# Kernel optimization log

Hardware: AMD Instinct MI355X
Metric: run time of the kernel (lower is better)

Reference implementation:

```python
import jax, jax.numpy as jnp
import numpy as np

B, N, D = 8, 2048, 256      # batch, tokens, model dim (= out_token_dims)
S = 128                     # query_key_dims
H = int(2.0 * D)            # expansion_factor * D = 512
EPS = 1e-5


def setup_inputs() -> dict:
    key = jax.random.key(0)
    ks = jax.random.split(key, 4)
    x = jax.random.normal(ks[0], (B, N, D), dtype=jnp.float32)
    g = jnp.ones((), jnp.float32)                                # ScaleNorm gain
    W_uv = jax.random.normal(ks[1], (D, 2 * H + S), jnp.float32) * 0.02
    b_uv = jnp.zeros((2 * H + S,), jnp.float32)
    gamma = jnp.ones((2, S), jnp.float32)                        # OffsetScale scale
    beta = jnp.zeros((2, S), jnp.float32)                        # OffsetScale offset
    W_o = jax.random.normal(ks[2], (H, D), jnp.float32) * 0.02
    b_o = jnp.zeros((D,), jnp.float32)
    return {"x": x, "g": g, "W_uv": W_uv, "b_uv": b_uv,
            "gamma": gamma, "beta": beta, "W_o": W_o, "b_o": b_o}


def reference(x, g, W_uv, b_uv, gamma, beta, W_o, b_o):
    d = x.shape[-1]
    # ScaleNorm: x / max(||x|| / sqrt(d), eps) * g
    norm = jnp.linalg.norm(x, axis=-1, keepdims=True) * jax.lax.rsqrt(jnp.float32(d))
    xn = x / jnp.maximum(norm, EPS) * g
    # fused uv projection + SiLU
    uv = jax.nn.silu(jnp.einsum('bnd,de->bne', xn, W_uv) + b_uv)
    u = uv[..., :H]            # gate branch        [B,N,H]
    v = uv[..., H:2 * H]       # value branch       [B,N,H]
    base = uv[..., 2 * H:]     # shared q/k base    [B,N,S]
    # OffsetScale heads=2 -> q, k (cheap per-dim affine)
    q = base * gamma[0] + beta[0]
    k = base * gamma[1] + beta[1]
    # single-head scores + ReLU^2 attention activation
    qk = jnp.einsum('bns,bms->bnm', q, k) * jax.lax.rsqrt(jnp.float32(S))
    attn = jnp.square(jax.nn.relu(qk))
    # gate * (attn @ v), then output projection back to D
    gated = u * jnp.einsum('bnm,bmh->bnh', attn, v)
    return jnp.einsum('bnh,hd->bnd', gated, W_o) + b_o
```

## Files before the change

kernel.cpp:

```cpp
#include <hip/hip_runtime.h>
#include <math.h>

#define BB 8
#define NN 2048
#define DD 256
#define SS 128
#define HH 512
#define EE 1152

typedef short bf16x8 __attribute__((ext_vector_type(8)));
typedef float f32x4 __attribute__((ext_vector_type(4)));

__device__ __forceinline__ short f2bf(float f) {
    union { float f; unsigned u; } a; a.f = f;
    unsigned r = a.u + 0x7FFFu + ((a.u >> 16) & 1u);
    return (short)(r >> 16);
}
__device__ __forceinline__ float bf2f(short s) {
    union { unsigned u; float f; } a; a.u = ((unsigned)(unsigned short)s) << 16;
    return a.f;
}
__device__ __forceinline__ void gl_lds16(const short* g, short* l) {
    __builtin_amdgcn_global_load_lds(
        (const __attribute__((address_space(1))) void*)g,
        (__attribute__((address_space(3))) void*)l, 16, 0, 0);
}

__global__ __launch_bounds__(256) void k_pre(
        const float* __restrict__ x, const float* __restrict__ gp,
        short* __restrict__ xn,
        const float* __restrict__ Wuv, const float* __restrict__ Wo,
        short* __restrict__ Wuv_t, short* __restrict__ Wo_t) {
    __shared__ float tile[32][33];
    int bid = blockIdx.x;
    int t = threadIdx.x;
    if (bid < 4096) {
        int wave = t >> 6, lane = t & 63;
        long row = (long)bid * 4 + wave;
        float4 xv = ((const float4*)(x + row * DD))[lane];
        float ss = xv.x*xv.x + xv.y*xv.y + xv.z*xv.z + xv.w*xv.w;
        #pragma unroll
        for (int off = 32; off > 0; off >>= 1) ss += __shfl_down(ss, off);
        ss = __shfl(ss, 0);
        float norm = sqrtf(ss) * 0.0625f;
        float scale = gp[0] / fmaxf(norm, 1e-5f);
        short4 o;
        o.x = f2bf(xv.x * scale); o.y = f2bf(xv.y * scale);
        o.z = f2bf(xv.z * scale); o.w = f2bf(xv.w * scale);
        ((short4*)(xn + row * DD))[lane] = o;
    } else if (bid < 4384) {
        int bid2 = bid - 4096;
        int et = bid2 % 36, dt = bid2 / 36;
        #pragma unroll
        for (int i = 0; i < 4; i++) {
            int idx = t + i*256, r = idx >> 5, c = idx & 31;
            tile[r][c] = Wuv[(long)(dt*32 + r)*EE + et*32 + c];
        }
        __syncthreads();
        #pragma unroll
        for (int i = 0; i < 4; i++) {
            int idx = t + i*256, r = idx >> 5, c = idx & 31;
            Wuv_t[(long)(et*32 + r)*DD + dt*32 + c] = f2bf(tile[c][r]);
        }
    } else {
        int bid3 = bid - 4384;
        int ht = bid3 % 16, dt = bid3 / 16;
        #pragma unroll
        for (int i = 0; i < 4; i++) {
            int idx = t + i*256, r = idx >> 5, c = idx & 31;
            tile[r][c] = Wo[(long)(ht*32 + r)*DD + dt*32 + c];
        }
        __syncthreads();
        #pragma unroll
        for (int i = 0; i < 4; i++) {
            int idx = t + i*256, r = idx >> 5, c = idx & 31;
            Wo_t[(long)(dt*32 + r)*HH + ht*32 + c] = f2bf(tile[c][r]);
        }
    }
}

__global__ __launch_bounds__(256) void k_gemm1(
        const short* __restrict__ xn, const short* __restrict__ Wuv_t,
        const float* __restrict__ b_uv,
        const float* __restrict__ gamma, const float* __restrict__ beta,
        short* __restrict__ u, short* __restrict__ v,
        short* __restrict__ q, short* __restrict__ k) {
    __shared__ short As[128*64];
    __shared__ short Bs[128*64];
    int m0 = blockIdx.x * 128, n0 = blockIdx.y * 128;
    int t = threadIdx.x, w = t >> 6, lane = t & 63;
    int wr = w & 1, wc = w >> 1, l16 = lane & 15, quad = lane >> 4;
    int lr = lane >> 3, lc = (lane & 7) * 8;
    f32x4 acc[4][4] = {};
    for (int k0 = 0; k0 < DD; k0 += 64) {
        __syncthreads();
        #pragma unroll
        for (int i = 0; i < 4; i++) {
            int r0 = i*32 + w*8;
            gl_lds16(&xn[(long)(m0 + r0 + lr)*DD + k0 + lc], &As[r0*64]);
            gl_lds16(&Wuv_t[(long)(n0 + r0 + lr)*DD + k0 + lc], &Bs[r0*64]);
        }
        __syncthreads();
        #pragma unroll
        for (int kk = 0; kk < 2; kk++) {
            bf16x8 a[4], bb[4];
            #pragma unroll
            for (int mt = 0; mt < 4; mt++)
                a[mt] = *(const bf16x8*)&As[(wr*64 + mt*16 + l16)*64 + kk*32 + quad*8];
            #pragma unroll
            for (int nt = 0; nt < 4; nt++)
                bb[nt] = *(const bf16x8*)&Bs[(wc*64 + nt*16 + l16)*64 + kk*32 + quad*8];
            #pragma unroll
            for (int mt = 0; mt < 4; mt++)
                #pragma unroll
                for (int nt = 0; nt < 4; nt++)
                    acc[mt][nt] = __builtin_amdgcn_mfma_f32_16x16x32_bf16(
                        a[mt], bb[nt], acc[mt][nt], 0,0,0);
        }
    }
    #pragma unroll
    for (int mt = 0; mt < 4; mt++)
    #pragma unroll
    for (int nt = 0; nt < 4; nt++)
    #pragma unroll
    for (int r = 0; r < 4; r++) {
        int gm = m0 + wr*64 + mt*16 + quad*4 + r;
        int ge = n0 + wc*64 + nt*16 + l16;
        float val = acc[mt][nt][r] + b_uv[ge];
        val = val / (1.0f + __expf(-val));
        if (ge < HH) {
            u[(long)gm*HH + ge] = f2bf(val);
        } else if (ge < 2*HH) {
            v[(long)gm*HH + (ge - HH)] = f2bf(val);
        } else {
            int si = ge - 2*HH;
            q[(long)gm*SS + si] = f2bf(val * gamma[si]      + beta[si]);
            k[(long)gm*SS + si] = f2bf(val * gamma[SS + si] + beta[SS + si]);
        }
    }
}

__global__ __launch_bounds__(256) void k_vfrag(
        const short* __restrict__ v, short* __restrict__ vfrag) {
    __shared__ short tile[32][520];
    int mt = blockIdx.x, b = blockIdx.y;
    int t = threadIdx.x;
    const short* vb = v + ((long)b * NN + mt * 32) * HH;
    #pragma unroll
    for (int i = 0; i < 8; i++) {
        int c = t + i * 256, r = c >> 6, co = (c & 63) * 8;
        *(bf16x8*)&tile[r][co] = *(const bf16x8*)&vb[(long)r * HH + co];
    }
    __syncthreads();
    short* dstb = vfrag + (((long)b * 64 + mt) * 32) * 512;
    #pragma unroll
    for (int i = 0; i < 8; i++) {
        int c = t + i * 256, ht = c >> 6, l = c & 63;
        int quad = l >> 4, l16 = l & 15;
        bf16x8 o;
        #pragma unroll
        for (int e = 0; e < 8; e++) o[e] = tile[quad*8 + e][ht*16 + l16];
        *(bf16x8*)&dstb[(long)ht * 512 + l * 8] = o;
    }
}

__global__ __launch_bounds__(512, 2) void k_attn(
        const short* __restrict__ q, const short* __restrict__ k,
        const short* __restrict__ vfrag, const short* __restrict__ u,
        short* __restrict__ gated) {
    __shared__ short ks[2][2][32][136];
    __shared__ short Ps[2][2][64][40];
    int b = blockIdx.x & 7;
    int i0 = (blockIdx.x >> 3) * 64;
    int t = threadIdx.x, w = t >> 6, lane = t & 63;
    int l16 = lane & 15, quad = lane >> 4;
    int qt = w >> 1, mt = w & 1;
    const short* qb  = q + ((long)b * NN + i0) * SS;
    const short* kb  = k + (long)b * NN * SS;
    const short* vfb = vfrag + (long)b * 64 * 32 * 512;
    const float RS = 0.08838834764831845f;

    int krow = t >> 4, kch = (t & 15) * 8;

    bf16x8 qf[4];
    #pragma unroll
    for (int kc = 0; kc < 4; kc++)
        qf[kc] = *(const bf16x8*)&qb[(long)(qt*16 + l16)*SS + kc*32 + quad*8];

    *(bf16x8*)&ks[0][0][krow][kch] = *(const bf16x8*)&kb[(long)krow*SS + kch];
    *(bf16x8*)&ks[0][1][krow][kch] = *(const bf16x8*)&kb[(long)(32 + krow)*SS + kch];
    bf16x8 kpre0 = *(const bf16x8*)&kb[(long)(64 + krow)*SS + kch];
    bf16x8 kpre1 = *(const bf16x8*)&kb[(long)(96 + krow)*SS + kch];
    bf16x8 vfc[8];
    #pragma unroll
    for (int jj = 0; jj < 4; jj++) {
        vfc[jj]     = *(const bf16x8*)&vfb[((long)(w*4 + jj))*512 + lane*8];
        vfc[4 + jj] = *(const bf16x8*)&vfb[((long)(32 + w*4 + jj))*512 + lane*8];
    }
    __syncthreads();

    f32x4 acc[16] = {};
    for (int s = 0; s < 32; s++) {
        int p = s & 1;
        int sk = (s + 2 < 32) ? s + 2 : s;
        bf16x8 kfar0 = *(const bf16x8*)&kb[(long)(sk*64 + krow)*SS + kch];
        bf16x8 kfar1 = *(const bf16x8*)&kb[(long)(sk*64 + 32 + krow)*SS + kch];
        int sv = (s + 1 < 32) ? s + 1 : s;
        bf16x8 vfn[8];
        #pragma unroll
        for (int jj = 0; jj < 4; jj++) {
            vfn[jj]     = *(const bf16x8*)&vfb[((long)(2*sv)*32     + w*4 + jj)*512 + lane*8];
            vfn[4 + jj] = *(const bf16x8*)&vfb[((long)(2*sv + 1)*32 + w*4 + jj)*512 + lane*8];
        }
        f32x4 scA = {}, scB = {};
        #pragma unroll
        for (int kc = 0; kc < 4; kc++) {
            bf16x8 kfA = *(const bf16x8*)&ks[p][0][mt*16 + l16][kc*32 + quad*8];
            scA = __builtin_amdgcn_mfma_f32_16x16x32_bf16(kfA, qf[kc], scA, 0,0,0);
        }
        #pragma unroll
        for (int kc = 0; kc < 4; kc++) {
            bf16x8 kfB = *(const bf16x8*)&ks[p][1][mt*16 + l16][kc*32 + quad*8];
            scB = __builtin_amdgcn_mfma_f32_16x16x32_bf16(kfB, qf[kc], scB, 0,0,0);
        }
        short4 pwA, pwB;
        {
            float a0 = fmaxf(scA[0]*RS, 0.f), a1 = fmaxf(scA[1]*RS, 0.f);
            float a2 = fmaxf(scA[2]*RS, 0.f), a3 = fmaxf(scA[3]*RS, 0.f);
            pwA.x = f2bf(a0*a0); pwA.y = f2bf(a1*a1);
            pwA.z = f2bf(a2*a2); pwA.w = f2bf(a3*a3);
            float b0 = fmaxf(scB[0]*RS, 0.f), b1 = fmaxf(scB[1]*RS, 0.f);
            float b2 = fmaxf(scB[2]*RS, 0.f), b3 = fmaxf(scB[3]*RS, 0.f);
            pwB.x = f2bf(b0*b0); pwB.y = f2bf(b1*b1);
            pwB.z = f2bf(b2*b2); pwB.w = f2bf(b3*b3);
        }
        *(short4*)&Ps[p][0][qt*16 + l16][mt*16 + quad*4] = pwA;
        *(short4*)&Ps[p][1][qt*16 + l16][mt*16 + quad*4] = pwB;
        *(bf16x8*)&ks[p^1][0][krow][kch] = kpre0;
        *(bf16x8*)&ks[p^1][1][krow][kch] = kpre1;
        kpre0 = kfar0; kpre1 = kfar1;
        __syncthreads();
        #pragma unroll
        for (int qq2 = 0; qq2 < 4; qq2++) {
            bf16x8 afA = *(const bf16x8*)&Ps[p][0][qq2*16 + l16][quad*8];
            #pragma unroll
            for (int jj = 0; jj < 4; jj++)
                acc[qq2*4 + jj] = __builtin_amdgcn_mfma_f32_16x16x32_bf16(
                    afA, vfc[jj], acc[qq2*4 + jj], 0,0,0);
        }
        #pragma unroll
        for (int qq2 = 0; qq2 < 4; qq2++) {
            bf16x8 afB = *(const bf16x8*)&Ps[p][1][qq2*16 + l16][quad*8];
            #pragma unroll
            for (int jj = 0; jj < 4; jj++)
                acc[qq2*4 + jj] = __builtin_amdgcn_mfma_f32_16x16x32_bf16(
                    afB, vfc[4 + jj], acc[qq2*4 + jj], 0,0,0);
        }
        #pragma unroll
        for (int i = 0; i < 8; i++) vfc[i] = vfn[i];
    }

    long rowbase = (long)b * NN + i0;
    #pragma unroll
    for (int qq2 = 0; qq2 < 4; qq2++)
    #pragma unroll
    for (int jj = 0; jj < 4; jj++) {
        int gh = (w*4 + jj)*16 + l16;
        #pragma unroll
        for (int r = 0; r < 4; r++) {
            long grow = rowbase + qq2*16 + quad*4 + r;
            float uval = bf2f(u[grow * HH + gh]);
            gated[grow * HH + gh] = f2bf(acc[qq2*4 + jj][r] * uval);
        }
    }
}

__global__ __launch_bounds__(256) void k_gemm2(
        const short* __restrict__ gated, const short* __restrict__ Wo_t,
        const float* __restrict__ b_o, float* __restrict__ out) {
    __shared__ short As[128*64];
    __shared__ short Bs[128*64];
    int m0 = blockIdx.x * 128, n0 = blockIdx.y * 128;
    int t = threadIdx.x, w = t >> 6, lane = t & 63;
    int wr = w & 1, wc = w >> 1, l16 = lane & 15, quad = lane >> 4;
    int lr = lane >> 3, lc = (lane & 7) * 8;
    f32x4 acc[4][4] = {};
    for (int k0 = 0; k0 < HH; k0 += 64) {
        __syncthreads();
        #pragma unroll
        for (int i = 0; i < 4; i++) {
            int r0 = i*32 + w*8;
            gl_lds16(&gated[(long)(m0 + r0 + lr)*HH + k0 + lc], &As[r0*64]);
            gl_lds16(&Wo_t[(long)(n0 + r0 + lr)*HH + k0 + lc], &Bs[r0*64]);
        }
        __syncthreads();
        #pragma unroll
        for (int kk = 0; kk < 2; kk++) {
            bf16x8 a[4], bb[4];
            #pragma unroll
            for (int mt = 0; mt < 4; mt++)
                a[mt] = *(const bf16x8*)&As[(wr*64 + mt*16 + l16)*64 + kk*32 + quad*8];
            #pragma unroll
            for (int nt = 0; nt < 4; nt++)
                bb[nt] = *(const bf16x8*)&Bs[(wc*64 + nt*16 + l16)*64 + kk*32 + quad*8];
            #pragma unroll
            for (int mt = 0; mt < 4; mt++)
                #pragma unroll
                for (int nt = 0; nt < 4; nt++)
                    acc[mt][nt] = __builtin_amdgcn_mfma_f32_16x16x32_bf16(
                        a[mt], bb[nt], acc[mt][nt], 0,0,0);
        }
    }
    #pragma unroll
    for (int mt = 0; mt < 4; mt++)
    #pragma unroll
    for (int nt = 0; nt < 4; nt++)
    #pragma unroll
    for (int r = 0; r < 4; r++) {
        int gm = m0 + wr*64 + mt*16 + quad*4 + r;
        int gd = n0 + wc*64 + nt*16 + l16;
        out[(long)gm*DD + gd] = acc[mt][nt][r] + b_o[gd];
    }
}

extern "C" void kernel_launch(void* const* d_in, const int* in_sizes, int n_in,
                              void* d_out, int out_size, void* d_ws, size_t ws_size,
                              hipStream_t stream) {
    const float* x     = (const float*)d_in[0];
    const float* g     = (const float*)d_in[1];
    const float* Wuv   = (const float*)d_in[2];
    const float* b_uv  = (const float*)d_in[3];
    const float* gamma = (const float*)d_in[4];
    const float* beta  = (const float*)d_in[5];
    const float* Wo    = (const float*)d_in[6];
    const float* b_o   = (const float*)d_in[7];
    float* out = (float*)d_out;

    short* ws    = (short*)d_ws;
    short* xn    = ws;
    short* Wuv_t = xn    + (long)16384 * 256;
    short* Wo_t  = Wuv_t + (long)1152 * 256;
    short* u     = Wo_t  + (long)256 * 512;
    short* v     = u     + (long)16384 * 512;
    short* vfrag = v     + (long)16384 * 512;
    short* qq    = vfrag + (long)16384 * 512;
    short* kk    = qq    + (long)16384 * 128;
    short* gated = kk    + (long)16384 * 128;

    k_pre<<<4512, 256, 0, stream>>>(x, g, xn, Wuv, Wo, Wuv_t, Wo_t);
    k_gemm1<<<dim3(128, 9), 256, 0, stream>>>(xn, Wuv_t, b_uv, gamma, beta, u, v, qq, kk);
    k_vfrag<<<dim3(64, 8), 256, 0, stream>>>(v, vfrag);
    k_attn<<<256, 512, 0, stream>>>(qq, kk, vfrag, u, gated);
    k_gemm2<<<dim3(128, 2), 256, 0, stream>>>(gated, Wo_t, b_o, out);
}
```

Before: 182.3 us.

## Fuse V fragment layout into gemm1 and output projection into attention kernel

```diff
diff --git a/kernel.cpp b/kernel.cpp
--- a/kernel.cpp
+++ b/kernel.cpp
@@ -83,7 +83,7 @@
         const short* __restrict__ xn, const short* __restrict__ Wuv_t,
         const float* __restrict__ b_uv,
         const float* __restrict__ gamma, const float* __restrict__ beta,
-        short* __restrict__ u, short* __restrict__ v,
+        short* __restrict__ u, short* __restrict__ vfrag,
         short* __restrict__ q, short* __restrict__ k) {
     __shared__ short As[128*64];
     __shared__ short Bs[128*64];
@@ -121,55 +121,49 @@
     #pragma unroll
     for (int mt = 0; mt < 4; mt++)
     #pragma unroll
-    for (int nt = 0; nt < 4; nt++)
-    #pragma unroll
-    for (int r = 0; r < 4; r++) {
-        int gm = m0 + wr*64 + mt*16 + quad*4 + r;
-        int ge = n0 + wc*64 + nt*16 + l16;
-        float val = acc[mt][nt][r] + b_uv[ge];
-        val = val / (1.0f + __expf(-val));
+    for (int nt = 0; nt < 4; nt++) {
+        int gm0 = m0 + wr*64 + mt*16 + quad*4;
+        int ge  = n0 + wc*64 + nt*16 + l16;
+        float val[4];
+        #pragma unroll
+        for (int r = 0; r < 4; r++) {
+            float xv = acc[mt][nt][r] + b_uv[ge];
+            val[r] = xv / (1.0f + __expf(-xv));
+        }
         if (ge < HH) {
-            u[(long)gm*HH + ge] = f2bf(val);
+            #pragma unroll
+            for (int r = 0; r < 4; r++)
+                u[(long)(gm0 + r)*HH + ge] = f2bf(val[r]);
         } else if (ge < 2*HH) {
-            v[(long)gm*HH + (ge - HH)] = f2bf(val);
+            int h = ge - HH;
+            long base = (((long)((gm0 >> 11)*64 + ((gm0 & 2047) >> 5)) * 32)
+                         + (h >> 4)) * 512
+                        + ((((gm0 & 31) >> 3)*16 + (h & 15)) * 8) + (gm0 & 7);
+            short4 o;
+            o.x = f2bf(val[0]); o.y = f2bf(val[1]);
+            o.z = f2bf(val[2]); o.w = f2bf(val[3]);
+            *(short4*)&vfrag[base] = o;
         } else {
             int si = ge - 2*HH;
-            q[(long)gm*SS + si] = f2bf(val * gamma[si]      + beta[si]);
-            k[(long)gm*SS + si] = f2bf(val * gamma[SS + si] + beta[SS + si]);
-        }
-    }
-}
-
-__global__ __launch_bounds__(256) void k_vfrag(
-        const short* __restrict__ v, short* __restrict__ vfrag) {
-    __shared__ short tile[32][520];
-    int mt = blockIdx.x, b = blockIdx.y;
-    int t = threadIdx.x;
-    const short* vb = v + ((long)b * NN + mt * 32) * HH;
-    #pragma unroll
-    for (int i = 0; i < 8; i++) {
-        int c = t + i * 256, r = c >> 6, co = (c & 63) * 8;
-        *(bf16x8*)&tile[r][co] = *(const bf16x8*)&vb[(long)r * HH + co];
-    }
-    __syncthreads();
-    short* dstb = vfrag + (((long)b * 64 + mt) * 32) * 512;
-    #pragma unroll
-    for (int i = 0; i < 8; i++) {
-        int c = t + i * 256, ht = c >> 6, l = c & 63;
-        int quad = l >> 4, l16 = l & 15;
-        bf16x8 o;
-        #pragma unroll
-        for (int e = 0; e < 8; e++) o[e] = tile[quad*8 + e][ht*16 + l16];
-        *(bf16x8*)&dstb[(long)ht * 512 + l * 8] = o;
-    }
-}
+            #pragma unroll
+            for (int r = 0; r < 4; r++) {
+                q[(long)(gm0 + r)*SS + si] = f2bf(val[r] * gamma[si]      + beta[si]);
+                k[(long)(gm0 + r)*SS + si] = f2bf(val[r] * gamma[SS + si] + beta[SS + si]);
+            }
+        }
+    }
+}
+
+#define KS(p,row)  (smem + ((p)*32 + (row))*136)
+#define PS(p,row)  (smem + 8704 + ((p)*64 + (row))*40)
+#define GT(hf,row) (smem + (hf)*16896 + (row)*264)
 
 __global__ __launch_bounds__(512, 2) void k_attn(
         const short* __restrict__ q, const short* __restrict__ k,
         const short* __restrict__ vfrag, const short* __restrict__ u,
-        short* __restrict__ gated) {
-    __shared__ short ks[2][2][32][136];
-    __shared__ short Ps[2][2][64][40];
+        const short* __restrict__ Wo_t, const float* __restrict__ b_o,
+        float* __restrict__ out) {
+    extern __shared__ __align__(16) short smem[];
     int b = blockIdx.x & 7;
     int i0 = (blockIdx.x >> 3) * 64;
     int t = threadIdx.x, w = t >> 6, lane = t & 63;
@@ -187,139 +181,99 @@
     for (int kc = 0; kc < 4; kc++)
         qf[kc] = *(const bf16x8*)&qb[(long)(qt*16 + l16)*SS + kc*32 + quad*8];
 
-    *(bf16x8*)&ks[0][0][krow][kch] = *(const bf16x8*)&kb[(long)krow*SS + kch];
-    *(bf16x8*)&ks[0][1][krow][kch] = *(const bf16x8*)&kb[(long)(32 + krow)*SS + kch];
-    bf16x8 kpre0 = *(const bf16x8*)&kb[(long)(64 + krow)*SS + kch];
-    bf16x8 kpre1 = *(const bf16x8*)&kb[(long)(96 + krow)*SS + kch];
-    bf16x8 vfc[8];
-    #pragma unroll
-    for (int jj = 0; jj < 4; jj++) {
-        vfc[jj]     = *(const bf16x8*)&vfb[((long)(w*4 + jj))*512 + lane*8];
-        vfc[4 + jj] = *(const bf16x8*)&vfb[((long)(32 + w*4 + jj))*512 + lane*8];
-    }
+    *(bf16x8*)&KS(0,krow)[kch] = *(const bf16x8*)&kb[(long)krow*SS + kch];
+    bf16x8 kpre = *(const bf16x8*)&kb[(long)(32 + krow)*SS + kch];
     __syncthreads();
 
     f32x4 acc[16] = {};
-    for (int s = 0; s < 32; s++) {
-        int p = s & 1;
-        int sk = (s + 2 < 32) ? s + 2 : s;
-        bf16x8 kfar0 = *(const bf16x8*)&kb[(long)(sk*64 + krow)*SS + kch];
-        bf16x8 kfar1 = *(const bf16x8*)&kb[(long)(sk*64 + 32 + krow)*SS + kch];
-        int sv = (s + 1 < 32) ? s + 1 : s;
-        bf16x8 vfn[8];
+    for (int it = 0; it < NN/32; it++) {
+        int p = it & 1;
+        int m0 = it * 32;
+        int mnext = (m0 + 64 < NN) ? m0 + 64 : m0;
+        bf16x8 knext = *(const bf16x8*)&kb[(long)(mnext + krow)*SS + kch];
+        bf16x8 vf[4];
+        #pragma unroll
+        for (int jj = 0; jj < 4; jj++)
+            vf[jj] = *(const bf16x8*)&vfb[((long)it*32 + (w*4 + jj))*512 + lane*8];
+        f32x4 sc = {};
+        #pragma unroll
+        for (int kc = 0; kc < 4; kc++) {
+            bf16x8 kf = *(const bf16x8*)&KS(p, mt*16 + l16)[kc*32 + quad*8];
+            sc = __builtin_amdgcn_mfma_f32_16x16x32_bf16(kf, qf[kc], sc, 0,0,0);
+        }
+        short4 pw;
+        {
+            float s0 = fmaxf(sc[0]*RS, 0.f), s1 = fmaxf(sc[1]*RS, 0.f);
+            float s2 = fmaxf(sc[2]*RS, 0.f), s3 = fmaxf(sc[3]*RS, 0.f);
+            pw.x = f2bf(s0*s0); pw.y = f2bf(s1*s1);
+            pw.z = f2bf(s2*s2); pw.w = f2bf(s3*s3);
+        }
+        *(short4*)&PS(p, qt*16 + l16)[mt*16 + quad*4] = pw;
+        *(bf16x8*)&KS(p^1, krow)[kch] = kpre;
+        kpre = knext;
+        __syncthreads();
+        bf16x8 af[4];
+        #pragma unroll
+        for (int qq2 = 0; qq2 < 4; qq2++)
+            af[qq2] = *(const bf16x8*)&PS(p, qq2*16 + l16)[quad*8];
+        #pragma unroll
+        for (int jj = 0; jj < 4; jj++)
+            #pragma unroll
+            for (int qq2 = 0; qq2 < 4; qq2++)
+                acc[qq2*4 + jj] = __builtin_amdgcn_mfma_f32_16x16x32_bf16(
+                    af[qq2], vf[jj], acc[qq2*4 + jj], 0,0,0);
+    }
+
+    long rowbase = (long)b * NN + i0;
+    __syncthreads();
+    {
+        int hf = w >> 2;
+        int hbase = (w & 3) * 64;
+        #pragma unroll
+        for (int qq2 = 0; qq2 < 4; qq2++)
         #pragma unroll
         for (int jj = 0; jj < 4; jj++) {
-            vfn[jj]     = *(const bf16x8*)&vfb[((long)(2*sv)*32     + w*4 + jj)*512 + lane*8];
-            vfn[4 + jj] = *(const bf16x8*)&vfb[((long)(2*sv + 1)*32 + w*4 + jj)*512 + lane*8];
-        }
-        f32x4 scA = {}, scB = {};
-        #pragma unroll
-        for (int kc = 0; kc < 4; kc++) {
-            bf16x8 kfA = *(const bf16x8*)&ks[p][0][mt*16 + l16][kc*32 + quad*8];
-            scA = __builtin_amdgcn_mfma_f32_16x16x32_bf16(kfA, qf[kc], scA, 0,0,0);
-        }
-        #pragma unroll
-        for (int kc = 0; kc < 4; kc++) {
-            bf16x8 kfB = *(const bf16x8*)&ks[p][1][mt*16 + l16][kc*32 + quad*8];
-            scB = __builtin_amdgcn_mfma_f32_16x16x32_bf16(kfB, qf[kc], scB, 0,0,0);
-        }
-        short4 pwA, pwB;
-        {
-            float a0 = fmaxf(scA[0]*RS, 0.f), a1 = fmaxf(scA[1]*RS, 0.f);
-            float a2 = fmaxf(scA[2]*RS, 0.f), a3 = fmaxf(scA[3]*RS, 0.f);
-            pwA.x = f2bf(a0*a0); pwA.y = f2bf(a1*a1);
-            pwA.z = f2bf(a2*a2); pwA.w = f2bf(a3*a3);
-            float b0 = fmaxf(scB[0]*RS, 0.f), b1 = fmaxf(scB[1]*RS, 0.f);
-            float b2 = fmaxf(scB[2]*RS, 0.f), b3 = fmaxf(scB[3]*RS, 0.f);
-            pwB.x = f2bf(b0*b0); pwB.y = f2bf(b1*b1);
-            pwB.z = f2bf(b2*b2); pwB.w = f2bf(b3*b3);
-        }
-        *(short4*)&Ps[p][0][qt*16 + l16][mt*16 + quad*4] = pwA;
-        *(short4*)&Ps[p][1][qt*16 + l16][mt*16 + quad*4] = pwB;
-        *(bf16x8*)&ks[p^1][0][krow][kch] = kpre0;
-        *(bf16x8*)&ks[p^1][1][krow][kch] = kpre1;
-        kpre0 = kfar0; kpre1 = kfar1;
-        __syncthreads();
-        #pragma unroll
-        for (int qq2 = 0; qq2 < 4; qq2++) {
-            bf16x8 afA = *(const bf16x8*)&Ps[p][0][qq2*16 + l16][quad*8];
-            #pragma unroll
-            for (int jj = 0; jj < 4; jj++)
-                acc[qq2*4 + jj] = __builtin_amdgcn_mfma_f32_16x16x32_bf16(
-                    afA, vfc[jj], acc[qq2*4 + jj], 0,0,0);
-        }
-        #pragma unroll
-        for (int qq2 = 0; qq2 < 4; qq2++) {
-            bf16x8 afB = *(const bf16x8*)&Ps[p][1][qq2*16 + l16][quad*8];
-            #pragma unroll
-            for (int jj = 0; jj < 4; jj++)
-                acc[qq2*4 + jj] = __builtin_amdgcn_mfma_f32_16x16x32_bf16(
-                    afB, vfc[4 + jj], acc[qq2*4 + jj], 0,0,0);
-        }
-        #pragma unroll
-        for (int i = 0; i < 8; i++) vfc[i] = vfn[i];
-    }
-
-    long rowbase = (long)b * NN + i0;
-    #pragma unroll
-    for (int qq2 = 0; qq2 < 4; qq2++)
-    #pragma unroll
-    for (int jj = 0; jj < 4; jj++) {
-        int gh = (w*4 + jj)*16 + l16;
-        #pragma unroll
-        for (int r = 0; r < 4; r++) {
-            long grow = rowbase + qq2*16 + quad*4 + r;
-            float uval = bf2f(u[grow * HH + gh]);
-            gated[grow * HH + gh] = f2bf(acc[qq2*4 + jj][r] * uval);
-        }
-    }
-}
-
-__global__ __launch_bounds__(256) void k_gemm2(
-        const short* __restrict__ gated, const short* __restrict__ Wo_t,
-        const float* __restrict__ b_o, float* __restrict__ out) {
-    __shared__ short As[128*64];
-    __shared__ short Bs[128*64];
-    int m0 = blockIdx.x * 128, n0 = blockIdx.y * 128;
-    int t = threadIdx.x, w = t >> 6, lane = t & 63;
-    int wr = w & 1, wc = w >> 1, l16 = lane & 15, quad = lane >> 4;
-    int lr = lane >> 3, lc = (lane & 7) * 8;
-    f32x4 acc[4][4] = {};
-    for (int k0 = 0; k0 < HH; k0 += 64) {
-        __syncthreads();
-        #pragma unroll
-        for (int i = 0; i < 4; i++) {
-            int r0 = i*32 + w*8;
-            gl_lds16(&gated[(long)(m0 + r0 + lr)*HH + k0 + lc], &As[r0*64]);
-            gl_lds16(&Wo_t[(long)(n0 + r0 + lr)*HH + k0 + lc], &Bs[r0*64]);
-        }
-        __syncthreads();
-        #pragma unroll
-        for (int kk = 0; kk < 2; kk++) {
-            bf16x8 a[4], bb[4];
-            #pragma unroll
-            for (int mt = 0; mt < 4; mt++)
-                a[mt] = *(const bf16x8*)&As[(wr*64 + mt*16 + l16)*64 + kk*32 + quad*8];
-            #pragma unroll
-            for (int nt = 0; nt < 4; nt++)
-                bb[nt] = *(const bf16x8*)&Bs[(wc*64 + nt*16 + l16)*64 + kk*32 + quad*8];
-            #pragma unroll
-            for (int mt = 0; mt < 4; mt++)
+            int gh = w*64 + jj*16 + l16;
+            #pragma unroll
+            for (int r = 0; r < 4; r++) {
+                long grow = rowbase + qq2*16 + quad*4 + r;
+                float uval = bf2f(u[grow*HH + gh]);
+                GT(hf, qq2*16 + quad*4 + r)[hbase + jj*16 + l16] =
+                    f2bf(acc[qq2*4 + jj][r] * uval);
+            }
+        }
+    }
+    __syncthreads();
+    f32x4 acc2[4][2] = {};
+    #pragma unroll
+    for (int p = 0; p < 2; p++) {
+        #pragma unroll
+        for (int kc = 0; kc < 8; kc++) {
+            bf16x8 A[4], Bf[2];
+            #pragma unroll
+            for (int mt2 = 0; mt2 < 4; mt2++)
+                A[mt2] = *(const bf16x8*)&GT(p, mt2*16 + l16)[kc*32 + quad*8];
+            #pragma unroll
+            for (int nt = 0; nt < 2; nt++)
+                Bf[nt] = *(const bf16x8*)&Wo_t[(long)(w*32 + nt*16 + l16)*HH
+                                               + p*256 + kc*32 + quad*8];
+            #pragma unroll
+            for (int mt2 = 0; mt2 < 4; mt2++)
                 #pragma unroll
-                for (int nt = 0; nt < 4; nt++)
-                    acc[mt][nt] = __builtin_amdgcn_mfma_f32_16x16x32_bf16(
-                        a[mt], bb[nt], acc[mt][nt], 0,0,0);
-        }
-    }
-    #pragma unroll
-    for (int mt = 0; mt < 4; mt++)
-    #pragma unroll
-    for (int nt = 0; nt < 4; nt++)
+                for (int nt = 0; nt < 2; nt++)
+                    acc2[mt2][nt] = __builtin_amdgcn_mfma_f32_16x16x32_bf16(
+                        A[mt2], Bf[nt], acc2[mt2][nt], 0,0,0);
+        }
+    }
+    #pragma unroll
+    for (int mt2 = 0; mt2 < 4; mt2++)
+    #pragma unroll
+    for (int nt = 0; nt < 2; nt++)
     #pragma unroll
     for (int r = 0; r < 4; r++) {
-        int gm = m0 + wr*64 + mt*16 + quad*4 + r;
-        int gd = n0 + wc*64 + nt*16 + l16;
-        out[(long)gm*DD + gd] = acc[mt][nt][r] + b_o[gd];
+        long grow = rowbase + mt2*16 + quad*4 + r;
+        int gd = w*32 + nt*16 + l16;
+        out[grow*DD + gd] = acc2[mt2][nt][r] + b_o[gd];
     }
 }
 
@@ -341,15 +295,12 @@
     short* Wuv_t = xn    + (long)16384 * 256;
     short* Wo_t  = Wuv_t + (long)1152 * 256;
     short* u     = Wo_t  + (long)256 * 512;
-    short* v     = u     + (long)16384 * 512;
-    short* vfrag = v     + (long)16384 * 512;
+    short* vfrag = u     + (long)16384 * 512;
     short* qq    = vfrag + (long)16384 * 512;
     short* kk    = qq    + (long)16384 * 128;
-    short* gated = kk    + (long)16384 * 128;
 
     k_pre<<<4512, 256, 0, stream>>>(x, g, xn, Wuv, Wo, Wuv_t, Wo_t);
-    k_gemm1<<<dim3(128, 9), 256, 0, stream>>>(xn, Wuv_t, b_uv, gamma, beta, u, v, qq, kk);
-    k_vfrag<<<dim3(64, 8), 256, 0, stream>>>(v, vfrag);
-    k_attn<<<256, 512, 0, stream>>>(qq, kk, vfrag, u, gated);
-    k_gemm2<<<dim3(128, 2), 256, 0, stream>>>(gated, Wo_t, b_o, out);
-}
+    k_gemm1<<<dim3(128, 9), 256, 0, stream>>>(xn, Wuv_t, b_uv, gamma, beta,
+                                              u, vfrag, qq, kk);
+    k_attn<<<256, 512, 67584, stream>>>(qq, kk, vfrag, u, Wo_t, b_o, out);
+}
```

Measured after the change: 163.7 us. 1.11x faster.
